# Kernel tuning notes

Hardware: AMD Instinct MI355X
Metric: run time of the kernel (lower is better)

## Reference

```python
import jax, jax.numpy as jnp
import numpy as np

KERNEL_MUL = 2.0
KERNEL_NUM = 5


def setup_inputs() -> dict:
    key = jax.random.key(0)
    k1, k2 = jax.random.split(key)
    source = jax.random.normal(k1, (4096, 256), dtype=jnp.float32)
    target = jax.random.normal(k2, (4096, 256), dtype=jnp.float32)
    return {"source": source, "target": target}


def _mmd(source, target):
    b = source.shape[0]
    total = jnp.concatenate([source, target], axis=0)  # [N, D], N = 2b
    n = total.shape[0]
    sq = jnp.sum(total * total, axis=-1)               # [N]
    gram = total @ total.T                             # [N, N]
    L2 = sq[:, None] + sq[None, :] - 2.0 * gram        # [N, N]
    # Data-dependent bandwidth (original uses .data -> no grad through it)
    bandwidth = jax.lax.stop_gradient(jnp.sum(L2) / (n * n - n))
    # Multi-bandwidth RBF kernel, averaged over KERNEL_NUM geometric sigmas.
    kernels = jnp.zeros_like(L2)
    for i in range(KERNEL_NUM):
        sigma = bandwidth * (KERNEL_MUL ** i)
        kernels = kernels + jnp.exp(-L2 / sigma)
    kernels = kernels / KERNEL_NUM
    XX = kernels[:b, :b]
    YY = kernels[b:, b:]
    XY = kernels[:b, b:]
    YX = kernels[b:, :b]
    return jnp.mean(XX + YY - XY - YX)


def reference(source, target):
    return _mmd(source, target)
```

## Files before the change

### kernel.cpp

```cpp
#include <hip/hip_runtime.h>
#include <hip/hip_bf16.h>

#define N_TOTAL 8192
#define B_HALF  4096
#define D       256
#define BM      128
#define NTILES  (N_TOTAL / BM)
#define NBLK    (NTILES * (NTILES + 1) / 2)
#define PREP_BLOCKS (N_TOTAL / 32)

typedef __bf16 bf16x8v __attribute__((ext_vector_type(8)));
typedef float  f32x4v  __attribute__((ext_vector_type(4)));

__device__ __forceinline__ unsigned short f2bf(float x) {
    unsigned int u = __float_as_uint(x);
    return (unsigned short)((u + 0x7FFFu + ((u >> 16) & 1u)) >> 16);
}
__device__ __forceinline__ float bf2f(unsigned short b) {
    return __uint_as_float(((unsigned int)b) << 16);
}

__global__ void prep_kernel(const float* __restrict__ src,
                            const float* __restrict__ tgt,
                            unsigned short* __restrict__ tb2,
                            float* __restrict__ sq,
                            float* __restrict__ colsum_part,
                            double* __restrict__ sumsq_part)
{
    __shared__ float colpart[4][256];
    __shared__ double wsum[4];
    int tid = threadIdx.x;
    int wv = tid >> 6, ln = tid & 63;
    int row0 = blockIdx.x * 32 + wv * 8;

    float cp0 = 0.f, cp1 = 0.f, cp2 = 0.f, cp3 = 0.f;
    double dsum = 0.0;

    for (int t = 0; t < 8; ++t) {
        int row = row0 + t;
        const float* p = (row < B_HALF) ? (src + (size_t)row * D)
                                        : (tgt + (size_t)(row - B_HALF) * D);
        float4 v = *(const float4*)(p + ln * 4);
        unsigned short b0 = f2bf(v.x), b1 = f2bf(v.y), b2 = f2bf(v.z), b3 = f2bf(v.w);
        float x0 = bf2f(b0), x1 = bf2f(b1), x2 = bf2f(b2), x3 = bf2f(b3);
        ushort4 u; u.x = b0; u.y = b1; u.z = b2; u.w = b3;
        *(ushort4*)(tb2 + ((size_t)(ln >> 1) * N_TOTAL + row) * 8 + (ln & 1) * 4) = u;

        cp0 += x0; cp1 += x1; cp2 += x2; cp3 += x3;

        float sqp = x0 * x0 + x1 * x1 + x2 * x2 + x3 * x3;
        #pragma unroll
        for (int off = 32; off; off >>= 1) sqp += __shfl_down(sqp, off, 64);
        if (ln == 0) { sq[row] = sqp; dsum += (double)sqp; }
    }
    colpart[wv][ln * 4 + 0] = cp0;
    colpart[wv][ln * 4 + 1] = cp1;
    colpart[wv][ln * 4 + 2] = cp2;
    colpart[wv][ln * 4 + 3] = cp3;
    if (ln == 0) wsum[wv] = dsum;
    __syncthreads();
    colsum_part[blockIdx.x * 256 + tid] =
        colpart[0][tid] + colpart[1][tid] + colpart[2][tid] + colpart[3][tid];
    if (tid == 0)
        sumsq_part[blockIdx.x] = wsum[0] + wsum[1] + wsum[2] + wsum[3];
}

__global__ void bw_kernel(const float* __restrict__ colsum_part,
                          const double* __restrict__ sumsq_part,
                          float* __restrict__ cexp) {
    __shared__ double red1[256], red2[256];
    int tid = threadIdx.x;
    float cs = 0.f;
    #pragma unroll 8
    for (int b = 0; b < PREP_BLOCKS; ++b)
        cs += colsum_part[b * 256 + tid];
    red1[tid] = sumsq_part[tid];
    red2[tid] = (double)cs * (double)cs;
    __syncthreads();
    for (int off = 128; off; off >>= 1) {
        if (tid < off) { red1[tid] += red1[tid + off]; red2[tid] += red2[tid + off]; }
        __syncthreads();
    }
    if (tid == 0) {
        double sl2 = 2.0 * (double)N_TOTAL * red1[0] - 2.0 * red2[0];
        double bw = sl2 / ((double)N_TOTAL * N_TOTAL - (double)N_TOTAL);
        cexp[0] = (float)(1.4426950408889634 / (16.0 * bw));
    }
}

__global__ __launch_bounds__(256)
void mmd_kernel(const unsigned short* __restrict__ tb2,
                const float* __restrict__ sq,
                const float* __restrict__ cexp_p,
                double* __restrict__ partials) {
    __shared__ float sqi[BM], sqj[BM];
    __shared__ float redbuf[4];

    int t = blockIdx.x;
    int r = (int)((sqrtf(8.0f * (float)t + 1.0f) - 1.0f) * 0.5f);
    while ((r + 1) * (r + 2) / 2 <= t) ++r;
    while (r * (r + 1) / 2 > t) --r;
    int c = t - r * (r + 1) / 2;
    int rowBase = r * BM, colBase = c * BM;

    int tid = threadIdx.x;
    int wv = tid >> 6, ln = tid & 63;
    int wr = wv >> 1, wc = wv & 1;
    int lo = ln & 15, hi = ln >> 4;

    if (tid < BM) sqi[tid] = sq[rowBase + tid];
    else          sqj[tid - BM] = sq[colBase + (tid - BM)];
    float cexp = cexp_p[0];
    __syncthreads();

    const char* pa = (const char*)tb2 +
        ((size_t)hi * N_TOTAL + rowBase + wr * 64 + lo) * 16;
    const char* pb = (const char*)tb2 +
        ((size_t)hi * N_TOTAL + colBase + wc * 64 + lo) * 16;
    const size_t KKSTRIDE = (size_t)4 * N_TOTAL * 16;

    f32x4v acc[4][4] = {};
    bf16x8v a[2][4], b[2][4];

    #pragma unroll
    for (int mi = 0; mi < 4; ++mi) a[0][mi] = *(const bf16x8v*)(pa + mi * 256);
    #pragma unroll
    for (int ni = 0; ni < 4; ++ni) b[0][ni] = *(const bf16x8v*)(pb + ni * 256);

    #pragma unroll
    for (int kk = 0; kk < 8; ++kk) {
        const int cur = kk & 1, nxt = cur ^ 1;
        if (kk < 7) {
            const char* qa = pa + (size_t)(kk + 1) * KKSTRIDE;
            const char* qb = pb + (size_t)(kk + 1) * KKSTRIDE;
            #pragma unroll
            for (int mi = 0; mi < 4; ++mi)
                a[nxt][mi] = *(const bf16x8v*)(qa + mi * 256);
            #pragma unroll
            for (int ni = 0; ni < 4; ++ni)
                b[nxt][ni] = *(const bf16x8v*)(qb + ni * 256);
        }
        #pragma unroll
        for (int mi = 0; mi < 4; ++mi)
            #pragma unroll
            for (int ni = 0; ni < 4; ++ni)
                acc[mi][ni] = __builtin_amdgcn_mfma_f32_16x16x32_bf16(
                    a[cur][mi], b[cur][ni], acc[mi][ni], 0, 0, 0);
    }

    float tacc = 0.f;
    #pragma unroll
    for (int mi = 0; mi < 4; ++mi) {
        float si4[4];
        #pragma unroll
        for (int rg = 0; rg < 4; ++rg)
            si4[rg] = sqi[wr * 64 + mi * 16 + hi * 4 + rg];
        #pragma unroll
        for (int ni = 0; ni < 4; ++ni) {
            float sj = sqj[wc * 64 + ni * 16 + lo];
            #pragma unroll
            for (int rg = 0; rg < 4; ++rg) {
                float arg = (2.0f * acc[mi][ni][rg] - (si4[rg] + sj)) * cexp;
                float e0 = __builtin_amdgcn_exp2f(arg);
                float e2 = e0 * e0, e4 = e2 * e2, e8 = e4 * e4, e16 = e8 * e8;
                tacc += (e0 + e2) + ((e4 + e8) + e16);
            }
        }
    }
    float w = ((r < NTILES / 2) == (c < NTILES / 2)) ? 1.f : -1.f;
    if (r != c) w *= 2.f;
    tacc *= w;

    #pragma unroll
    for (int off = 32; off; off >>= 1) tacc += __shfl_down(tacc, off, 64);
    if (ln == 0) redbuf[wv] = tacc;
    __syncthreads();
    if (tid == 0)
        partials[blockIdx.x] =
            (double)(redbuf[0] + redbuf[1] + redbuf[2] + redbuf[3]);
}

__global__ void final_kernel(const double* __restrict__ partials,
                             float* __restrict__ out) {
    __shared__ double dred[256];
    int tid = threadIdx.x;
    double d = 0.0;
    for (int i = tid; i < NBLK; i += 256) d += partials[i];
    dred[tid] = d;
    __syncthreads();
    for (int off = 128; off; off >>= 1) {
        if (tid < off) dred[tid] += dred[tid + off];
        __syncthreads();
    }
    if (tid == 0)
        out[0] = (float)(dred[0] / (5.0 * (double)B_HALF * (double)B_HALF));
}

extern "C" void kernel_launch(void* const* d_in, const int* in_sizes, int n_in,
                              void* d_out, int out_size, void* d_ws, size_t ws_size,
                              hipStream_t stream) {
    const float* src = (const float*)d_in[0];
    const float* tgt = (const float*)d_in[1];
    float* out = (float*)d_out;
    char* ws = (char*)d_ws;

    float*  cexp     = (float*)(ws + 16);
    double* ssqpart  = (double*)(ws + 2048);
    float*  sq       = (float*)(ws + 4096);
    double* partials = (double*)(ws + 36864);
    float*  cspart   = (float*)(ws + 131072);
    unsigned short* tb2 = (unsigned short*)(ws + 1048576);

    prep_kernel<<<PREP_BLOCKS, 256, 0, stream>>>(src, tgt, tb2, sq, cspart,
                                                 ssqpart);
    bw_kernel<<<1, 256, 0, stream>>>(cspart, ssqpart, cexp);
    mmd_kernel<<<NBLK, 256, 0, stream>>>(tb2, sq, cexp, partials);
    final_kernel<<<1, 256, 0, stream>>>(partials, out);
}
```

Before: 59.85 us.

## Drop register double-buffering, raise occupancy, prescale norms, fuse epilogue FMA

Removes the explicit two-stage register prefetch of the A/B fragments and adds a min-blocks-per-CU hint of 4. The aim is to cut VGPR pressure so more waves can hide load latency, instead of relying on intra-wave prefetch. MFMA bursts are wrapped in s_setprio so compute-ready waves get issue priority. The squared norms are pre-multiplied by the exponent scale when loaded to shared memory, so the epilogue becomes a single FMA per element. The risk is that each wave now stalls on its own loads when occupancy does not actually rise enough to cover the latency.

```diff
diff --git a/kernel.cpp b/kernel.cpp
--- a/kernel.cpp
+++ b/kernel.cpp
@@ -88,7 +88,7 @@
     }
 }
 
-__global__ __launch_bounds__(256)
+__global__ __launch_bounds__(256, 4)
 void mmd_kernel(const unsigned short* __restrict__ tb2,
                 const float* __restrict__ sq,
                 const float* __restrict__ cexp_p,
@@ -108,9 +108,9 @@
     int wr = wv >> 1, wc = wv & 1;
     int lo = ln & 15, hi = ln >> 4;
 
-    if (tid < BM) sqi[tid] = sq[rowBase + tid];
-    else          sqj[tid - BM] = sq[colBase + (tid - BM)];
     float cexp = cexp_p[0];
+    if (tid < BM) sqi[tid] = sq[rowBase + tid] * cexp;
+    else          sqj[tid - BM] = sq[colBase + (tid - BM)] * cexp;
     __syncthreads();
 
     const char* pa = (const char*)tb2 +
@@ -120,34 +120,28 @@
     const size_t KKSTRIDE = (size_t)4 * N_TOTAL * 16;
 
     f32x4v acc[4][4] = {};
-    bf16x8v a[2][4], b[2][4];
-
-    #pragma unroll
-    for (int mi = 0; mi < 4; ++mi) a[0][mi] = *(const bf16x8v*)(pa + mi * 256);
-    #pragma unroll
-    for (int ni = 0; ni < 4; ++ni) b[0][ni] = *(const bf16x8v*)(pb + ni * 256);
 
     #pragma unroll
     for (int kk = 0; kk < 8; ++kk) {
-        const int cur = kk & 1, nxt = cur ^ 1;
-        if (kk < 7) {
-            const char* qa = pa + (size_t)(kk + 1) * KKSTRIDE;
-            const char* qb = pb + (size_t)(kk + 1) * KKSTRIDE;
-            #pragma unroll
-            for (int mi = 0; mi < 4; ++mi)
-                a[nxt][mi] = *(const bf16x8v*)(qa + mi * 256);
-            #pragma unroll
-            for (int ni = 0; ni < 4; ++ni)
-                b[nxt][ni] = *(const bf16x8v*)(qb + ni * 256);
-        }
+        bf16x8v a[4], b[4];
+        const char* qa = pa + (size_t)kk * KKSTRIDE;
+        const char* qb = pb + (size_t)kk * KKSTRIDE;
+        #pragma unroll
+        for (int mi = 0; mi < 4; ++mi) a[mi] = *(const bf16x8v*)(qa + mi * 256);
+        #pragma unroll
+        for (int ni = 0; ni < 4; ++ni) b[ni] = *(const bf16x8v*)(qb + ni * 256);
+
+        __builtin_amdgcn_s_setprio(1);
         #pragma unroll
         for (int mi = 0; mi < 4; ++mi)
             #pragma unroll
             for (int ni = 0; ni < 4; ++ni)
                 acc[mi][ni] = __builtin_amdgcn_mfma_f32_16x16x32_bf16(
-                    a[cur][mi], b[cur][ni], acc[mi][ni], 0, 0, 0);
-    }
-
+                    a[mi], b[ni], acc[mi][ni], 0, 0, 0);
+        __builtin_amdgcn_s_setprio(0);
+    }
+
+    float c2 = 2.0f * cexp;
     float tacc = 0.f;
     #pragma unroll
     for (int mi = 0; mi < 4; ++mi) {
@@ -158,9 +152,12 @@
         #pragma unroll
         for (int ni = 0; ni < 4; ++ni) {
             float sj = sqj[wc * 64 + ni * 16 + lo];
+            float ss[4];
+            #pragma unroll
+            for (int rg = 0; rg < 4; ++rg) ss[rg] = si4[rg] + sj;
             #pragma unroll
             for (int rg = 0; rg < 4; ++rg) {
-                float arg = (2.0f * acc[mi][ni][rg] - (si4[rg] + sj)) * cexp;
+                float arg = __builtin_fmaf(acc[mi][ni][rg], c2, -ss[rg]);
                 float e0 = __builtin_amdgcn_exp2f(arg);
                 float e2 = e0 * e0, e4 = e2 * e2, e8 = e4 * e4, e16 = e8 * e8;
                 tacc += (e0 + e2) + ((e4 + e8) + e16);
```

New measurement: 58.76 us. No clear change (-1.8%).
